# Kernel tuning notes

Measured on AMD Instinct MI355X. Metric: run time of the kernel, lower is better.

The kernel has to match this reference:

```python
import jax, jax.numpy as jnp
import numpy as np

N_NODES = 10000
N_EDGES = 100000
F_NODE = 128
F_EDGE = 16
HEADS = 8
OUT_CH = 128  # per-head channels in PyG TransformerConv
HC = HEADS * OUT_CH


def setup_inputs() -> dict:
    key = jax.random.key(0)
    ks = jax.random.split(key, 12)
    sN = 1.0 / np.sqrt(F_NODE)
    sE = 1.0 / np.sqrt(F_EDGE)
    return {
        "x": jax.random.normal(ks[0], (N_NODES, F_NODE), dtype=jnp.float32),
        "edge_attr": jax.random.normal(ks[1], (N_EDGES, F_EDGE), dtype=jnp.float32),
        "edge_index": jax.random.randint(ks[2], (2, N_EDGES), 0, N_NODES, dtype=jnp.int32),
        "Wq": jax.random.normal(ks[3], (F_NODE, HC), dtype=jnp.float32) * sN,
        "bq": jnp.zeros((HC,), dtype=jnp.float32),
        "Wk": jax.random.normal(ks[4], (F_NODE, HC), dtype=jnp.float32) * sN,
        "bk": jnp.zeros((HC,), dtype=jnp.float32),
        "Wv": jax.random.normal(ks[5], (F_NODE, HC), dtype=jnp.float32) * sN,
        "bv": jnp.zeros((HC,), dtype=jnp.float32),
        "We": jax.random.normal(ks[6], (F_EDGE, HC), dtype=jnp.float32) * sE,  # lin_edge has no bias in PyG
        "Wskip": jax.random.normal(ks[7], (F_NODE, OUT_CH), dtype=jnp.float32) * sN,
        "bskip": jnp.zeros((OUT_CH,), dtype=jnp.float32),
        "Wd": jax.random.normal(ks[8], (OUT_CH, 1), dtype=jnp.float32) * (1.0 / np.sqrt(OUT_CH)),
        "bd": jnp.zeros((1,), dtype=jnp.float32),
    }


def reference(x, edge_attr, edge_index, Wq, bq, Wk, bk, Wv, bv, We, Wskip, bskip, Wd, bd):
    N = x.shape[0]
    src, dst = edge_index[0], edge_index[1]  # messages flow src -> dst

    q = (x @ Wq + bq).reshape(N, HEADS, OUT_CH)
    k = (x @ Wk + bk).reshape(N, HEADS, OUT_CH)
    v = (x @ Wv + bv).reshape(N, HEADS, OUT_CH)
    e = (edge_attr @ We).reshape(-1, HEADS, OUT_CH)  # [E, H, C]

    k_j = k[src] + e                        # [E, H, C]
    alpha = jnp.einsum("ehc,ehc->eh", q[dst], k_j) / np.sqrt(OUT_CH)  # [E, H]

    # segment softmax over destination node
    m = jax.ops.segment_max(alpha, dst, num_segments=N)   # [N, H]
    a = jnp.exp(alpha - m[dst])
    s = jax.ops.segment_sum(a, dst, num_segments=N)       # [N, H]
    alpha_n = a / (s[dst] + 1e-16)                        # [E, H]

    msg = (v[src] + e) * alpha_n[:, :, None]              # [E, H, C]
    out = jax.ops.segment_sum(msg, dst, num_segments=N)   # [N, H, C]

    out = out.mean(axis=1)                                # concat=False -> head average, [N, C]
    out = out + x @ Wskip + bskip                         # root/skip connection
    out = jax.nn.relu(out)
    # dropout is identity at inference
    pooled = out.sum(axis=0)                              # [C]
    return pooled @ Wd + bd                               # [1]
```

## Files before the change

kernel.cpp:

```cpp
#include <hip/hip_runtime.h>

#define N_NODES 10000
#define N_EDGES 100000
#define F_NODE 128
#define HEADS 8
#define HC 1024
#define NCOLS2 2432
#define NB2 (NCOLS2 / 128)
#define SLOT_CAP 48

typedef __attribute__((ext_vector_type(8))) short bf16x8;
typedef __attribute__((ext_vector_type(4))) float f32x4;
typedef __attribute__((ext_vector_type(2))) float f32x2;

__device__ __forceinline__ void atomAddF(float* p, float v) {
    unsafeAtomicAdd(p, v);
}
__device__ __forceinline__ unsigned short f2bf(float f) {
    union { float f; unsigned u; } c; c.f = f;
    unsigned u = c.u + 0x7fffu + ((c.u >> 16) & 1u);
    return (unsigned short)(u >> 16);
}
__device__ __forceinline__ float bLo(unsigned x) {
    union { unsigned u; float f; } c; c.u = x << 16; return c.f;
}
__device__ __forceinline__ float bHi(unsigned x) {
    union { unsigned u; float f; } c; c.u = x & 0xffff0000u; return c.f;
}
__device__ __forceinline__ float bf2f(unsigned short u) {
    union { unsigned u; float f; } c; c.u = ((unsigned)u) << 16; return c.f;
}
__device__ __forceinline__ unsigned pk4fp8(unsigned a, unsigned b) {
    int w = __builtin_amdgcn_cvt_pk_fp8_f32(bLo(a), bHi(a), 0, false);
    w = __builtin_amdgcn_cvt_pk_fp8_f32(bLo(b), bHi(b), w, true);
    return (unsigned)w;
}
__device__ __forceinline__ void dq16(uint4 q, float* f) {
    f32x2 p;
    p = __builtin_amdgcn_cvt_pk_f32_fp8(q.x, false); f[0] = p.x;  f[1] = p.y;
    p = __builtin_amdgcn_cvt_pk_f32_fp8(q.x, true);  f[2] = p.x;  f[3] = p.y;
    p = __builtin_amdgcn_cvt_pk_f32_fp8(q.y, false); f[4] = p.x;  f[5] = p.y;
    p = __builtin_amdgcn_cvt_pk_f32_fp8(q.y, true);  f[6] = p.x;  f[7] = p.y;
    p = __builtin_amdgcn_cvt_pk_f32_fp8(q.z, false); f[8] = p.x;  f[9] = p.y;
    p = __builtin_amdgcn_cvt_pk_f32_fp8(q.z, true);  f[10] = p.x; f[11] = p.y;
    p = __builtin_amdgcn_cvt_pk_f32_fp8(q.w, false); f[12] = p.x; f[13] = p.y;
    p = __builtin_amdgcn_cvt_pk_f32_fp8(q.w, true);  f[14] = p.x; f[15] = p.y;
}
__device__ __forceinline__ void edge_accum(
    uint4 xq4, uint4 vq4, float2 eav, float svv, bool valid,
    const float* gf, float qwx, float qwy, float du_r, float scale,
    float& s_reg, float& t0, float& t1, float* va) {
    float xq[16];
    dq16(xq4, xq);
    float d = eav.x * qwx + eav.y * qwy;
    #pragma unroll
    for (int j = 0; j < 16; ++j) d += gf[j] * xq[j];
    d += __shfl_xor(d, 1); d += __shfl_xor(d, 2); d += __shfl_xor(d, 4);
    float a = __expf((d + du_r + svv) * scale);
    a = valid ? a : 0.f;
    s_reg += a;
    t0 += a * eav.x; t1 += a * eav.y;
    float vq[16];
    dq16(vq4, vq);
    #pragma unroll
    for (int j = 0; j < 16; ++j) va[j] += a * vq[j];
}

#define PREP_A 1250
#define PREP_B (PREP_A + NCOLS2 / 2)
#define PREP_C (PREP_B + 10)
#define PREP_D (PREP_C + 64)
__global__ __launch_bounds__(256) void prep_all(
    const float* __restrict__ x, unsigned short* __restrict__ xb,
    unsigned* __restrict__ xf8, const int* __restrict__ ei,
    int* __restrict__ cnt, int2* __restrict__ slots,
    const float* __restrict__ Wq, const float* __restrict__ Wk,
    const float* __restrict__ Wv, const float* __restrict__ Wskip,
    const float* __restrict__ We, const float* __restrict__ bq,
    const float* __restrict__ bk, const float* __restrict__ bv,
    const float* __restrict__ bskip, unsigned short* __restrict__ wt,
    float* __restrict__ bias, unsigned short* __restrict__ w2t) {
    int tid = threadIdx.x;
    if (blockIdx.x < PREP_A) {
        int i = blockIdx.x * 256 + tid;
        float4 f = ((const float4*)x)[i];
        ushort4 o;
        o.x = f2bf(f.x); o.y = f2bf(f.y); o.z = f2bf(f.z); o.w = f2bf(f.w);
        ((ushort4*)xb)[i] = o;
        int w = __builtin_amdgcn_cvt_pk_fp8_f32(f.x, f.y, 0, false);
        w = __builtin_amdgcn_cvt_pk_fp8_f32(f.z, f.w, w, true);
        xf8[i] = (unsigned)w;
        if (i < N_EDGES) {
            int src = ei[i];
            int dst = ei[N_EDGES + i];
            int pos = atomicAdd(&cnt[dst], 1);
            if (pos < SLOT_CAP) slots[(size_t)dst * SLOT_CAP + pos] = make_int2(src, i);
        }
    } else if (blockIdx.x < PREP_B) {
        __shared__ float wesh[2][128];
        int bi = blockIdx.x - PREP_A;
        int cid = tid >> 7, d = tid & 127;
        int n = 2 * bi + cid;
        float val;
        if (n < 1024) {
            int h = n >> 7, f2 = n & 127;
            wesh[cid][d] = Wk[(size_t)f2 * HC + h * 128 + d];
            __syncthreads();
            const float* wq = Wq + (size_t)d * HC + h * 128;
            float s = 0.f;
            #pragma unroll
            for (int c = 0; c < 128; ++c) s += wq[c] * wesh[cid][c];
            val = s;
        } else if (n < 2048) {
            val = Wv[(size_t)d * HC + (n - 1024)];
        } else if (n < 2176) {
            val = Wskip[(size_t)d * 128 + (n - 2048)];
        } else if (n < 2304) {
            int hf = n - 2176, h = hf >> 4, f = hf & 15;
            wesh[cid][d] = We[(size_t)f * HC + h * 128 + d];
            __syncthreads();
            const float* wq = Wq + (size_t)d * HC + h * 128;
            float s = 0.f;
            #pragma unroll
            for (int c = 0; c < 128; ++c) s += wq[c] * wesh[cid][c];
            val = s;
        } else if (n < 2312) {
            int h = n - 2304;
            wesh[cid][d] = bk[h * 128 + d];
            __syncthreads();
            const float* wq = Wq + (size_t)d * HC + h * 128;
            float s = 0.f;
            #pragma unroll
            for (int c = 0; c < 128; ++c) s += wq[c] * wesh[cid][c];
            val = s;
        } else if (n < 2320) {
            int h = n - 2312;
            wesh[cid][d] = bq[h * 128 + d];
            __syncthreads();
            const float* wk = Wk + (size_t)d * HC + h * 128;
            float s = 0.f;
            #pragma unroll
            for (int c = 0; c < 128; ++c) s += wk[c] * wesh[cid][c];
            val = s;
        } else {
            val = 0.f;
        }
        wt[(size_t)n * 128 + d] = f2bf(val);
    } else if (blockIdx.x < PREP_C) {
        int n = (blockIdx.x - PREP_B) * 256 + tid;
        if (n >= NCOLS2) return;
        float val;
        if (n < 1024) val = 0.f;
        else if (n < 2048) val = bv[n - 1024];
        else if (n < 2176) val = bskip[n - 2048];
        else if (n < 2304) {
            int hf = n - 2176, h = hf >> 4, f = hf & 15;
            float s = 0.f;
            for (int c = 0; c < 128; ++c)
                s += bq[h * 128 + c] * We[(size_t)f * HC + h * 128 + c];
            val = s;
        } else if (n < 2312) {
            int h = n - 2304;
            float s = 0.f;
            for (int c = 0; c < 128; ++c) s += bq[h * 128 + c] * bk[h * 128 + c];
            val = s;
        } else val = 0.f;
        bias[n] = val;
    } else {
        int c = (blockIdx.x - PREP_C) * 2 + (tid >> 7);
        int d = tid & 127;
        int h = d >> 4, f = d & 15;
        w2t[(size_t)c * 128 + d] = f2bf(We[(size_t)f * HC + h * 128 + c] * 0.125f);
    }
}

__global__ __launch_bounds__(256) void gemm_mfma(
    const unsigned short* __restrict__ xb, const unsigned short* __restrict__ wt,
    const float* __restrict__ bias, unsigned char* __restrict__ xgf8,
    unsigned char* __restrict__ vf8, unsigned short* __restrict__ sqb,
    float* __restrict__ du, float* __restrict__ sv) {
    __shared__ unsigned short lds[18432];
    unsigned short (*As)[72] = (unsigned short(*)[72])lds;
    unsigned short (*Bs)[72] = (unsigned short(*)[72])(lds + 9216);
    int tid = threadIdx.x;
    int n0 = blockIdx.x * 128, m0 = blockIdx.y * 128;
    int w = tid >> 6, lane = tid & 63;
    int wm = (w >> 1) * 64, wn = (w & 1) * 64;
    int quad = lane >> 4, l16 = lane & 15;
    f32x4 acc[4][4];
    #pragma unroll
    for (int i = 0; i < 4; ++i)
        #pragma unroll
        for (int j = 0; j < 4; ++j) acc[i][j] = (f32x4){0.f, 0.f, 0.f, 0.f};

    for (int ko = 0; ko < 128; ko += 64) {
        #pragma unroll
        for (int tI = 0; tI < 4; ++tI) {
            int cId = tid + tI * 256;
            int r = cId >> 3, c8 = (cId & 7) << 3;
            int gr = m0 + r;
            uint4 av = make_uint4(0u, 0u, 0u, 0u);
            if (gr < N_NODES)
                av = *(const uint4*)(xb + (size_t)gr * 128 + ko + c8);
            *(uint4*)(&As[r][c8]) = av;
            *(uint4*)(&Bs[r][c8]) =
                *(const uint4*)(wt + (size_t)(n0 + r) * 128 + ko + c8);
        }
        __syncthreads();
        #pragma unroll
        for (int ks = 0; ks < 64; ks += 32) {
            bf16x8 a[4], b[4];
            #pragma unroll
            for (int mt = 0; mt < 4; ++mt)
                a[mt] = *(const bf16x8*)&As[wm + mt * 16 + l16][ks + quad * 8];
            #pragma unroll
            for (int nt = 0; nt < 4; ++nt)
                b[nt] = *(const bf16x8*)&Bs[wn + nt * 16 + l16][ks + quad * 8];
            #pragma unroll
            for (int mt = 0; mt < 4; ++mt)
                #pragma unroll
                for (int nt = 0; nt < 4; ++nt)
                    acc[mt][nt] = __builtin_amdgcn_mfma_f32_16x16x32_bf16(
                        a[mt], b[nt], acc[mt][nt], 0, 0, 0);
        }
        __syncthreads();
    }
    int nt0 = n0 >> 7;
    if (nt0 >= 16) {
        #pragma unroll
        for (int mt = 0; mt < 4; ++mt)
            #pragma unroll
            for (int r = 0; r < 4; ++r) {
                int row = m0 + wm + mt * 16 + quad * 4 + r;
                if (row >= N_NODES) continue;
                #pragma unroll
                for (int nt = 0; nt < 4; ++nt) {
                    int col = n0 + wn + nt * 16 + l16;
                    float val = acc[mt][nt][r] + bias[col];
                    if (col < 2304) {
                        sqb[(size_t)row * 256 + (col - 2048)] = f2bf(val);
                    } else if (col < 2312) {
                        du[(size_t)row * 8 + (col - 2304)] = val;
                    } else if (col < 2320) {
                        sv[(size_t)row * 8 + (col - 2312)] = val;
                    }
                }
            }
    } else {
        unsigned short* wst = lds + w * 4608;
        #pragma unroll
        for (int mt = 0; mt < 4; ++mt)
            #pragma unroll
            for (int r = 0; r < 4; ++r) {
                int rl = mt * 16 + quad * 4 + r;
                #pragma unroll
                for (int nt = 0; nt < 4; ++nt) {
                    int cl = nt * 16 + l16;
                    wst[rl * 72 + cl] = f2bf(acc[mt][nt][r] + bias[n0 + wn + cl]);
                }
            }
        unsigned char* dst = (nt0 < 8) ? xgf8 : vf8;
        int colbase = (n0 & 1023) + wn;
        #pragma unroll
        for (int p = 0; p < 4; ++p) {
            int rl = p * 16 + (lane >> 2);
            int row = m0 + wm + rl;
            if (row < N_NODES) {
                const uint4* sp = (const uint4*)(wst + rl * 72 + (lane & 3) * 16);
                uint4 u0 = sp[0], u1 = sp[1];
                uint4 o;
                o.x = pk4fp8(u0.x, u0.y);
                o.y = pk4fp8(u0.z, u0.w);
                o.z = pk4fp8(u1.x, u1.y);
                o.w = pk4fp8(u1.z, u1.w);
                *(uint4*)(dst + (size_t)row * 1024 + colbase + (lane & 3) * 16) = o;
            }
        }
    }
}

__global__ __launch_bounds__(256) void node_kernel(
    const unsigned char* __restrict__ xgf8, const unsigned char* __restrict__ xf8,
    const unsigned char* __restrict__ vf8, const unsigned short* __restrict__ sqb,
    const float* __restrict__ ea, const float* __restrict__ du,
    const float* __restrict__ sv, const int2* __restrict__ slots,
    const int* __restrict__ cnt, unsigned short* __restrict__ ttb,
    float* __restrict__ hsum) {
    __shared__ float lva[2][16][64];
    __shared__ float lst[2][3][64];
    int t = threadIdx.x;
    int w = t >> 6, lane = t & 63;
    int ns = w >> 1;
    int half = w & 1;
    int lh = lane & 7, h = lane >> 3;
    const float scale = 0.08838834764831845f;
    int n = blockIdx.x * 2 + ns;

    uint4 gq = *(const uint4*)(xgf8 + (size_t)n * 1024 + 16 * lane);
    float gf[16];
    dq16(gq, gf);
    ushort2 qwu = *(const ushort2*)(sqb + (size_t)n * 256 + 128 + h * 16 + 2 * lh);
    float qwx = bf2f(qwu.x), qwy = bf2f(qwu.y);
    float du_r = du[(size_t)n * 8 + h];

    int cn = cnt[n];
    cn = (cn > SLOT_CAP) ? SLOT_CAP : cn;
    int mid = (cn + 1) >> 1;
    int begin = half ? mid : 0;
    int end = half ? cn : mid;
    const int2* sp = slots + (size_t)n * SLOT_CAP;
    float va[16];
    #pragma unroll
    for (int i = 0; i < 16; ++i) va[i] = 0.f;
    float s_reg = 0.f, t0 = 0.f, t1 = 0.f;

    int2 saC = make_int2(0, 0), sbC = make_int2(0, 0);
    uint4 xAC, xBC, vAC, vBC;
    float2 eAC, eBC;
    float svAC = 0.f, svBC = 0.f;
    bool bBC = false;

    if (begin < end) {
        bool bv = (begin + 1 < end);
        int i1 = bv ? begin + 1 : begin;
        saC = sp[begin]; sbC = sp[i1]; bBC = bv;
        xAC = *(const uint4*)(xf8 + (size_t)saC.x * 128 + lh * 16);
        xBC = *(const uint4*)(xf8 + (size_t)sbC.x * 128 + lh * 16);
        vAC = *(const uint4*)(vf8 + (size_t)saC.x * 1024 + 16 * lane);
        vBC = *(const uint4*)(vf8 + (size_t)sbC.x * 1024 + 16 * lane);
        eAC = *(const float2*)(ea + (size_t)saC.y * 16 + 2 * lh);
        eBC = *(const float2*)(ea + (size_t)sbC.y * 16 + 2 * lh);
        svAC = sv[(size_t)saC.x * 8 + h];
        svBC = sv[(size_t)sbC.x * 8 + h];
    }
    for (int ii = begin; ii < end; ii += 2) {
        int in = ii + 2;
        bool hn = in < end;
        int2 saN = make_int2(0, 0), sbN = make_int2(0, 0);
        uint4 xAN, xBN, vAN, vBN;
        float2 eAN, eBN;
        float svAN = 0.f, svBN = 0.f;
        bool bBN = false;
        if (hn) {
            bool bv = (in + 1 < end);
            int i1 = bv ? in + 1 : in;
            saN = sp[in]; sbN = sp[i1]; bBN = bv;
            xAN = *(const uint4*)(xf8 + (size_t)saN.x * 128 + lh * 16);
            xBN = *(const uint4*)(xf8 + (size_t)sbN.x * 128 + lh * 16);
            vAN = *(const uint4*)(vf8 + (size_t)saN.x * 1024 + 16 * lane);
            vBN = *(const uint4*)(vf8 + (size_t)sbN.x * 1024 + 16 * lane);
            eAN = *(const float2*)(ea + (size_t)saN.y * 16 + 2 * lh);
            eBN = *(const float2*)(ea + (size_t)sbN.y * 16 + 2 * lh);
            svAN = sv[(size_t)saN.x * 8 + h];
            svBN = sv[(size_t)sbN.x * 8 + h];
        }
        edge_accum(xAC, vAC, eAC, svAC, true, gf, qwx, qwy, du_r, scale,
                   s_reg, t0, t1, va);
        edge_accum(xBC, vBC, eBC, svBC, bBC, gf, qwx, qwy, du_r, scale,
                   s_reg, t0, t1, va);
        if (hn) {
            saC = saN; sbC = sbN; bBC = bBN;
            xAC = xAN; xBC = xBN; vAC = vAN; vBC = vBN;
            eAC = eAN; eBC = eBN; svAC = svAN; svBC = svBN;
        }
    }
    if (half == 0) {
        #pragma unroll
        for (int i = 0; i < 16; ++i) lva[ns][i][lane] = va[i];
        lst[ns][0][lane] = s_reg;
        lst[ns][1][lane] = t0;
        lst[ns][2][lane] = t1;
    }
    __syncthreads();
    if (half == 1) {
        s_reg += lst[ns][0][lane];
        t0 += lst[ns][1][lane];
        t1 += lst[ns][2][lane];
        #pragma unroll
        for (int i = 0; i < 16; ++i) va[i] += lva[ns][i][lane];

        float inv = 1.f / (s_reg + 1e-16f);
        ushort2 tw;
        tw.x = f2bf(t0 * inv);
        tw.y = f2bf(t1 * inv);
        *(ushort2*)(ttb + (size_t)n * 128 + h * 16 + 2 * lh) = tw;
        float sc = inv * 0.125f;
        #pragma unroll
        for (int i = 0; i < 16; ++i) {
            float o = va[i] * sc;
            o += __shfl_xor(o, 8);
            o += __shfl_xor(o, 16);
            o += __shfl_xor(o, 32);
            va[i] = o;
        }
        if (lane < 8) {
            float* hp = hsum + (size_t)n * 128 + lane * 16;
            #pragma unroll
            for (int p2 = 0; p2 < 4; ++p2) {
                float4 h4 = make_float4(va[4 * p2], va[4 * p2 + 1],
                                        va[4 * p2 + 2], va[4 * p2 + 3]);
                ((float4*)hp)[p2] = h4;
            }
        }
    }
}

__global__ __launch_bounds__(256) void out_gemm(
    const unsigned short* __restrict__ ttb, const unsigned short* __restrict__ w2t,
    const float* __restrict__ hsum, const unsigned short* __restrict__ sqb,
    float* __restrict__ pooled, int* __restrict__ done,
    const float* __restrict__ Wd, const float* __restrict__ bd,
    float* __restrict__ out) {
    __shared__ unsigned short As[128][136];
    __shared__ float pool_sh[128];
    __shared__ int last_sh;
    int tid = threadIdx.x;
    int m0 = blockIdx.x * 128;
    int w = tid >> 6, lane = tid & 63;
    int wm = (w >> 1) * 64, wn = (w & 1) * 64;
    int quad = lane >> 4, l16 = lane & 15;
    if (tid < 128) pool_sh[tid] = 0.f;
    #pragma unroll
    for (int tI = 0; tI < 8; ++tI) {
        int cId = tid + tI * 256;
        int r = cId >> 4, c8 = (cId & 15) << 3;
        int gr = m0 + r;
        uint4 av = make_uint4(0u, 0u, 0u, 0u);
        if (gr < N_NODES)
            av = *(const uint4*)(ttb + (size_t)gr * 128 + c8);
        *(uint4*)(&As[r][c8]) = av;
    }
    __syncthreads();
    f32x4 acc[4][4];
    #pragma unroll
    for (int i = 0; i < 4; ++i)
        #pragma unroll
        for (int j = 0; j < 4; ++j) acc[i][j] = (f32x4){0.f, 0.f, 0.f, 0.f};

    const unsigned short* bb = w2t + (size_t)(wn + l16) * 128 + quad * 8;
    #pragma unroll
    for (int ks = 0; ks < 128; ks += 32) {
        bf16x8 a[4], b[4];
        #pragma unroll
        for (int mt = 0; mt < 4; ++mt)
            a[mt] = *(const bf16x8*)&As[wm + mt * 16 + l16][ks + quad * 8];
        #pragma unroll
        for (int nt = 0; nt < 4; ++nt)
            b[nt] = *(const bf16x8*)(bb + (size_t)nt * 16 * 128 + ks);
        #pragma unroll
        for (int mt = 0; mt < 4; ++mt)
            #pragma unroll
            for (int nt = 0; nt < 4; ++nt)
                acc[mt][nt] = __builtin_amdgcn_mfma_f32_16x16x32_bf16(
                    a[mt], b[nt], acc[mt][nt], 0, 0, 0);
    }
    float pl[4] = {0.f, 0.f, 0.f, 0.f};
    #pragma unroll
    for (int mt = 0; mt < 4; ++mt) {
        #pragma unroll
        for (int r = 0; r < 4; ++r) {
            int row = m0 + wm + mt * 16 + quad * 4 + r;
            if (row >= N_NODES) continue;
            #pragma unroll
            for (int nt = 0; nt < 4; ++nt) {
                int col = wn + nt * 16 + l16;
                float val = acc[mt][nt][r] + hsum[(size_t)row * 128 + col]
                            + bf2f(sqb[(size_t)row * 256 + col]);
                pl[nt] += fmaxf(val, 0.f);
            }
        }
    }
    #pragma unroll
    for (int nt = 0; nt < 4; ++nt)
        atomicAdd(&pool_sh[wn + nt * 16 + l16], pl[nt]);
    __syncthreads();
    if (tid < 128) atomAddF(&pooled[tid], pool_sh[tid]);
    __threadfence();
    if (tid == 0) last_sh = (atomicAdd(done, 1) == (int)gridDim.x - 1);
    __syncthreads();
    if (last_sh && tid < 64) {
        float p0 = __hip_atomic_load(&pooled[2 * tid], __ATOMIC_RELAXED,
                                     __HIP_MEMORY_SCOPE_AGENT);
        float p1 = __hip_atomic_load(&pooled[2 * tid + 1], __ATOMIC_RELAXED,
                                     __HIP_MEMORY_SCOPE_AGENT);
        float vv = p0 * Wd[2 * tid] + p1 * Wd[2 * tid + 1];
        vv += __shfl_xor(vv, 1);  vv += __shfl_xor(vv, 2);  vv += __shfl_xor(vv, 4);
        vv += __shfl_xor(vv, 8);  vv += __shfl_xor(vv, 16); vv += __shfl_xor(vv, 32);
        if (tid == 0) out[0] = vv + bd[0];
    }
}

extern "C" void kernel_launch(void* const* d_in, const int* in_sizes, int n_in,
                              void* d_out, int out_size, void* d_ws, size_t ws_size,
                              hipStream_t stream) {
    const float* x     = (const float*)d_in[0];
    const float* eattr = (const float*)d_in[1];
    const int*   ei    = (const int*)d_in[2];
    const float* Wq    = (const float*)d_in[3];
    const float* bq    = (const float*)d_in[4];
    const float* Wk    = (const float*)d_in[5];
    const float* bk    = (const float*)d_in[6];
    const float* Wv    = (const float*)d_in[7];
    const float* bv    = (const float*)d_in[8];
    const float* We    = (const float*)d_in[9];
    const float* Wskip = (const float*)d_in[10];
    const float* bskip = (const float*)d_in[11];
    const float* Wd    = (const float*)d_in[12];
    const float* bd    = (const float*)d_in[13];
    float* out = (float*)d_out;

    char* ws = (char*)d_ws;
    unsigned char*  xgf8 = (unsigned char*)(ws + 0);
    unsigned char*  vf8  = (unsigned char*)(ws + 10240000);
    unsigned short* sqb  = (unsigned short*)(ws + 20480000);
    float* hsum = (float*)(ws + 25600000);
    unsigned short* xb   = (unsigned short*)(ws + 30720000);
    unsigned short* ttb  = xb;
    unsigned*       xf8  = (unsigned*)(ws + 33280000);
    float* du   = (float*)(ws + 34560000);
    float* sv   = (float*)(ws + 34880000);
    unsigned short* wt   = (unsigned short*)(ws + 35200000);
    float* bias = (float*)(ws + 35822592);
    unsigned short* w2t  = (unsigned short*)(ws + 35832320);
    int* cnt    = (int*)(ws + 35865088);
    float* pooled = (float*)(ws + 35905088);
    int* done   = (int*)(ws + 35905600);
    int2* slots = (int2*)(ws + 35905616);

    hipMemsetAsync(cnt, 0, 40000 + 512 + 16, stream);

    prep_all<<<PREP_D, 256, 0, stream>>>(
        x, xb, xf8, ei, cnt, slots, Wq, Wk, Wv, Wskip, We, bq, bk, bv, bskip,
        wt, bias, w2t);

    gemm_mfma<<<dim3(NB2, (N_NODES + 127) / 128), 256, 0, stream>>>(
        xb, wt, bias, xgf8, vf8, sqb, du, sv);

    node_kernel<<<N_NODES / 2, 256, 0, stream>>>(
        xgf8, (const unsigned char*)xf8, vf8, sqb, eattr, du, sv, slots, cnt,
        ttb, hsum);

    out_gemm<<<(N_NODES + 127) / 128, 256, 0, stream>>>(
        ttb, w2t, hsum, sqb, pooled, done, Wd, bd, out);
}
```

Measured before the change: 192.7 us.

## Use one wave per node in node kernel; halve out_gemm row tile

The node kernel now gives each wavefront a whole destination node instead of splitting a node's edge list across two wavefronts. This removes the shared-memory partial-sum combine and the block-wide barrier, and puts four nodes in each block. Separately, out_gemm uses a 64-row tile instead of 128, which doubles its block count for more parallelism. The cost is that each wave walks its full edge list (about 10 edges on average) serially, which lengthens per-node latency and makes load balance depend on degree variance.

```diff
diff --git a/kernel.cpp b/kernel.cpp
--- a/kernel.cpp
+++ b/kernel.cpp
@@ -286,15 +286,11 @@
     const float* __restrict__ sv, const int2* __restrict__ slots,
     const int* __restrict__ cnt, unsigned short* __restrict__ ttb,
     float* __restrict__ hsum) {
-    __shared__ float lva[2][16][64];
-    __shared__ float lst[2][3][64];
     int t = threadIdx.x;
     int w = t >> 6, lane = t & 63;
-    int ns = w >> 1;
-    int half = w & 1;
     int lh = lane & 7, h = lane >> 3;
     const float scale = 0.08838834764831845f;
-    int n = blockIdx.x * 2 + ns;
+    int n = blockIdx.x * 4 + w;
 
     uint4 gq = *(const uint4*)(xgf8 + (size_t)n * 1024 + 16 * lane);
     float gf[16];
@@ -305,9 +301,7 @@
 
     int cn = cnt[n];
     cn = (cn > SLOT_CAP) ? SLOT_CAP : cn;
-    int mid = (cn + 1) >> 1;
-    int begin = half ? mid : 0;
-    int end = half ? cn : mid;
+    int end = cn;
     const int2* sp = slots + (size_t)n * SLOT_CAP;
     float va[16];
     #pragma unroll
@@ -320,10 +314,10 @@
     float svAC = 0.f, svBC = 0.f;
     bool bBC = false;
 
-    if (begin < end) {
-        bool bv = (begin + 1 < end);
-        int i1 = bv ? begin + 1 : begin;
-        saC = sp[begin]; sbC = sp[i1]; bBC = bv;
+    if (0 < end) {
+        bool bv = (1 < end);
+        int i1 = bv ? 1 : 0;
+        saC = sp[0]; sbC = sp[i1]; bBC = bv;
         xAC = *(const uint4*)(xf8 + (size_t)saC.x * 128 + lh * 16);
         xBC = *(const uint4*)(xf8 + (size_t)sbC.x * 128 + lh * 16);
         vAC = *(const uint4*)(vf8 + (size_t)saC.x * 1024 + 16 * lane);
@@ -333,7 +327,7 @@
         svAC = sv[(size_t)saC.x * 8 + h];
         svBC = sv[(size_t)sbC.x * 8 + h];
     }
-    for (int ii = begin; ii < end; ii += 2) {
+    for (int ii = 0; ii < end; ii += 2) {
         int in = ii + 2;
         bool hn = in < end;
         int2 saN = make_int2(0, 0), sbN = make_int2(0, 0);
@@ -364,43 +358,28 @@
             eAC = eAN; eBC = eBN; svAC = svAN; svBC = svBN;
         }
     }
-    if (half == 0) {
-        #pragma unroll
-        for (int i = 0; i < 16; ++i) lva[ns][i][lane] = va[i];
-        lst[ns][0][lane] = s_reg;
-        lst[ns][1][lane] = t0;
-        lst[ns][2][lane] = t1;
-    }
-    __syncthreads();
-    if (half == 1) {
-        s_reg += lst[ns][0][lane];
-        t0 += lst[ns][1][lane];
-        t1 += lst[ns][2][lane];
-        #pragma unroll
-        for (int i = 0; i < 16; ++i) va[i] += lva[ns][i][lane];
-
-        float inv = 1.f / (s_reg + 1e-16f);
-        ushort2 tw;
-        tw.x = f2bf(t0 * inv);
-        tw.y = f2bf(t1 * inv);
-        *(ushort2*)(ttb + (size_t)n * 128 + h * 16 + 2 * lh) = tw;
-        float sc = inv * 0.125f;
-        #pragma unroll
-        for (int i = 0; i < 16; ++i) {
-            float o = va[i] * sc;
-            o += __shfl_xor(o, 8);
-            o += __shfl_xor(o, 16);
-            o += __shfl_xor(o, 32);
-            va[i] = o;
-        }
-        if (lane < 8) {
-            float* hp = hsum + (size_t)n * 128 + lane * 16;
-            #pragma unroll
-            for (int p2 = 0; p2 < 4; ++p2) {
-                float4 h4 = make_float4(va[4 * p2], va[4 * p2 + 1],
-                                        va[4 * p2 + 2], va[4 * p2 + 3]);
-                ((float4*)hp)[p2] = h4;
-            }
+
+    float inv = 1.f / (s_reg + 1e-16f);
+    ushort2 tw;
+    tw.x = f2bf(t0 * inv);
+    tw.y = f2bf(t1 * inv);
+    *(ushort2*)(ttb + (size_t)n * 128 + h * 16 + 2 * lh) = tw;
+    float sc = inv * 0.125f;
+    #pragma unroll
+    for (int i = 0; i < 16; ++i) {
+        float o = va[i] * sc;
+        o += __shfl_xor(o, 8);
+        o += __shfl_xor(o, 16);
+        o += __shfl_xor(o, 32);
+        va[i] = o;
+    }
+    if (lane < 8) {
+        float* hp = hsum + (size_t)n * 128 + lane * 16;
+        #pragma unroll
+        for (int p2 = 0; p2 < 4; ++p2) {
+            float4 h4 = make_float4(va[4 * p2], va[4 * p2 + 1],
+                                    va[4 * p2 + 2], va[4 * p2 + 3]);
+            ((float4*)hp)[p2] = h4;
         }
     }
 }
@@ -411,17 +390,17 @@
     float* __restrict__ pooled, int* __restrict__ done,
     const float* __restrict__ Wd, const float* __restrict__ bd,
     float* __restrict__ out) {
-    __shared__ unsigned short As[128][136];
+    __shared__ unsigned short As[64][136];
     __shared__ float pool_sh[128];
     __shared__ int last_sh;
     int tid = threadIdx.x;
-    int m0 = blockIdx.x * 128;
+    int m0 = blockIdx.x * 64;
     int w = tid >> 6, lane = tid & 63;
-    int wm = (w >> 1) * 64, wn = (w & 1) * 64;
+    int wm = (w >> 1) * 32, wn = (w & 1) * 64;
     int quad = lane >> 4, l16 = lane & 15;
     if (tid < 128) pool_sh[tid] = 0.f;
     #pragma unroll
-    for (int tI = 0; tI < 8; ++tI) {
+    for (int tI = 0; tI < 4; ++tI) {
         int cId = tid + tI * 256;
         int r = cId >> 4, c8 = (cId & 15) << 3;
         int gr = m0 + r;
@@ -431,24 +410,24 @@
         *(uint4*)(&As[r][c8]) = av;
     }
     __syncthreads();
-    f32x4 acc[4][4];
-    #pragma unroll
-    for (int i = 0; i < 4; ++i)
+    f32x4 acc[2][4];
+    #pragma unroll
+    for (int i = 0; i < 2; ++i)
         #pragma unroll
         for (int j = 0; j < 4; ++j) acc[i][j] = (f32x4){0.f, 0.f, 0.f, 0.f};
 
     const unsigned short* bb = w2t + (size_t)(wn + l16) * 128 + quad * 8;
     #pragma unroll
     for (int ks = 0; ks < 128; ks += 32) {
-        bf16x8 a[4], b[4];
-        #pragma unroll
-        for (int mt = 0; mt < 4; ++mt)
+        bf16x8 a[2], b[4];
+        #pragma unroll
+        for (int mt = 0; mt < 2; ++mt)
             a[mt] = *(const bf16x8*)&As[wm + mt * 16 + l16][ks + quad * 8];
         #pragma unroll
         for (int nt = 0; nt < 4; ++nt)
             b[nt] = *(const bf16x8*)(bb + (size_t)nt * 16 * 128 + ks);
         #pragma unroll
-        for (int mt = 0; mt < 4; ++mt)
+        for (int mt = 0; mt < 2; ++mt)
             #pragma unroll
             for (int nt = 0; nt < 4; ++nt)
                 acc[mt][nt] = __builtin_amdgcn_mfma_f32_16x16x32_bf16(
@@ -456,7 +435,7 @@
     }
     float pl[4] = {0.f, 0.f, 0.f, 0.f};
     #pragma unroll
-    for (int mt = 0; mt < 4; ++mt) {
+    for (int mt = 0; mt < 2; ++mt) {
         #pragma unroll
         for (int r = 0; r < 4; ++r) {
             int row = m0 + wm + mt * 16 + quad * 4 + r;
@@ -536,10 +515,10 @@
     gemm_mfma<<<dim3(NB2, (N_NODES + 127) / 128), 256, 0, stream>>>(
         xb, wt, bias, xgf8, vf8, sqb, du, sv);
 
-    node_kernel<<<N_NODES / 2, 256, 0, stream>>>(
+    node_kernel<<<N_NODES / 4, 256, 0, stream>>>(
         xgf8, (const unsigned char*)xf8, vf8, sqb, eattr, du, sv, slots, cnt,
         ttb, hsum);
 
-    out_gemm<<<(N_NODES + 127) / 128, 256, 0, stream>>>(
+    out_gemm<<<(N_NODES + 63) / 64, 256, 0, stream>>>(
         ttb, w2t, hsum, sqb, pooled, done, Wd, bd, out);
 }
```

New measurement: 191.6 us. No clear change (-0.5%).
